# Kernel tuning notes

Hardware: AMD Instinct MI355X
Metric: run time of the kernel (lower is better)

Reference implementation:

```python
import jax, jax.numpy as jnp
import numpy as np

S = 4  # spixel_downsize


def _shift2d(x, oy, ox):
    # out[..., y, x] = x[..., y - oy, x - ox] if in-bounds else 0 (zero pad)
    pad = [(0, 0)] * (x.ndim - 2) + [(S, S), (S, S)]
    xp = jnp.pad(x, pad)
    h, w = x.shape[-2], x.shape[-1]
    return xp[..., S - oy:S - oy + h, S - ox:S - ox + w]


def _valid_mask(h, w, oy, ox):
    ys = jnp.arange(h)
    xs = jnp.arange(w)
    my = (ys - oy >= 0) & (ys - oy < h)
    mx = (xs - ox >= 0) & (xs - ox < w)
    return my[:, None] & mx[None, :]


def _conv3d(x, w, stride, pad):
    return jax.lax.conv_general_dilated(
        x, w, window_strides=stride, padding=[(p, p) for p in pad],
        dimension_numbers=('NCDHW', 'OIDHW', 'NCDHW'))


def _basic(x, w, stride, pad):
    # BasicConv: Conv3d(bias=False) + BN(identity at init) + ReLU
    return jax.nn.relu(_conv3d(x, w, stride, pad))


def setup_inputs() -> dict:
    key = jax.random.key(0)
    ks = jax.random.split(key, 8)
    cv = jax.random.normal(ks[0], (1, 8, 24, 128, 256), jnp.float32)
    sp = jax.random.uniform(ks[1], (1, 9, 128, 256), jnp.float32)
    xy = jax.random.normal(ks[2], (1, 2, 128, 256), jnp.float32)
    w_stem = jax.random.normal(ks[3], (16, 72, 1, 1, 1), jnp.float32) * 0.05
    w1a = jax.random.normal(ks[4], (32, 16, 3, 2, 2), jnp.float32) * 0.05
    w1b = jax.random.normal(ks[5], (32, 32, 3, 1, 1), jnp.float32) * 0.05
    w2a = jax.random.normal(ks[6], (64, 32, 3, 2, 2), jnp.float32) * 0.05
    w2b = jax.random.normal(ks[7], (64, 64, 3, 1, 1), jnp.float32) * 0.05
    return dict(cv=cv, sp=sp, xy=xy, w_stem=w_stem, w1a=w1a, w1b=w1b, w2a=w2a, w2b=w2b)


def reference(cv, sp, xy, w_stem, w1a, w1b, w2a, w2b):
    b, c, d, h, w = cv.shape
    feats, probs = [], []
    uv0 = jnp.zeros((b, 2, h, w), cv.dtype)
    # 9 shifted neighbors; neighbor k shifts by (S*((k//3)-1), S*((k%3)-1)).
    # All uv writes in the original target slot 0 and sequentially overwrite;
    for k in range(9):
        oy = S * ((k // 3) - 1)
        ox = S * ((k % 3) - 1)
        p = _shift2d(sp[:, k], oy, ox)                      # (b,h,w), zeros outside
        probs.append(p)
        feats.append(_shift2d(cv, oy, ox) * p[:, None, None])  # (b,c,d,h,w)
        u = _shift2d(xy, oy, ox) * p[:, None]               # (b,2,h,w)
        mask = _valid_mask(h, w, oy, ox)[None, None]
        uv0 = jnp.where(mask, u, uv0)
    # (b, c, 9, d, h, w) -> (b, 9c, d, h, w), matching torch reshape order
    feat = jnp.stack(feats, axis=2).reshape(b, c * 9, d, h, w)
    prob_sum = jnp.sum(jnp.stack(probs, axis=1), axis=1, keepdims=True)  # (b,1,h,w)
    tot = prob_sum.reshape(b, 1, h // S, S, w // S, S).mean((3, 5))      # avg_pool2d
    tot_up = jnp.repeat(jnp.repeat(tot, S, axis=2), S, axis=3)           # nearest upsample
    feat = feat / tot_up[:, :, None]                                     # (b,9c,d,h,w)
    feat = _basic(feat, w_stem, (1, 1, 1), (0, 0, 0))
    f1 = _basic(feat, w1a, (2, 2, 2), (1, 0, 0))
    f1 = _basic(f1, w1b, (1, 1, 1), (1, 0, 0))
    f2 = _basic(f1, w2a, (2, 2, 2), (1, 0, 0))
    f2 = _basic(f2, w2b, (1, 1, 1), (1, 0, 0))
    # uv.sum(2) == uv0 since only neighbor-slot 0 is written
    uv = uv0.reshape(b, 2, h // S, S, w // S, S).mean((3, 5)) / tot      # (b,2,h/S,w/S)
    return f1, f2, uv.reshape(b, 2, -1)
```

## Files before the change

### kernel.cpp

```cpp
#include <hip/hip_runtime.h>

#define HH 128
#define WW 256

#define OFF_TOT   0
#define OFF_WT    2048
#define WT_STEM   0
#define WT_1A     1152
#define WT_1B     7296
#define WT_2A     10368
#define WT_2B     34944
#define OFF_STEM  49280
#define OFF_F1A   12632192
#define OFF_F1N   15777920
#define OFF_F2A   49280

__global__ __launch_bounds__(256) void k_pre(
    const float* __restrict__ sp, const float* __restrict__ xy,
    const float* __restrict__ wstem, const float* __restrict__ w1a,
    const float* __restrict__ w1b, const float* __restrict__ w2a,
    const float* __restrict__ w2b,
    float* __restrict__ tot, float* __restrict__ uv_out, float* __restrict__ wt)
{
  int gid = blockIdx.x * 256 + threadIdx.x;
  if (gid < 1152) { int o = gid & 15, r = gid >> 4; int ci = r / 9, k = r - ci * 9;
    wt[WT_STEM + gid] = wstem[o * 72 + ci * 9 + k]; }
  if (gid < 6144) { int o = gid & 31, ci = (gid >> 5) & 15, tp = gid >> 9;
    wt[WT_1A + gid] = w1a[o * 192 + ci * 12 + tp]; }
  if (gid < 3072) { int o = gid & 31, ci = (gid >> 5) & 31, kd = gid >> 10;
    wt[WT_1B + gid] = w1b[(o * 32 + ci) * 3 + kd]; }
  if (gid < 24576) { int o = gid & 63, ci = (gid >> 6) & 31, tp = gid >> 11;
    wt[WT_2A + gid] = w2a[o * 384 + ci * 12 + tp]; }
  if (gid < 12288) { int o = gid & 63, ci = (gid >> 6) & 63, kd = gid >> 12;
    wt[WT_2B + gid] = w2b[(o * 64 + ci) * 3 + kd]; }
  if (gid < 8192) {
    int cell = gid >> 2, q = gid & 3;
    int Y = cell >> 6, X = cell & 63;
    float tsum = 0.f, u0 = 0.f, u1 = 0.f;
    int y = Y * 4 + q;
#pragma unroll
    for (int j = 0; j < 4; ++j) {
      int x = X * 4 + j;
      float psum = 0.f;
#pragma unroll
      for (int k = 0; k < 9; ++k) {
        int oy = 4 * ((k / 3) - 1), ox = 4 * ((k % 3) - 1);
        int sy = y - oy, sx = x - ox;
        if (sy >= 0 && sy < HH && sx >= 0 && sx < WW)
          psum += sp[k * HH * WW + sy * WW + sx];
      }
      tsum += psum;
      int oy = (y >= 4) ? 4 : 0;
      int ox = (x >= 4) ? 4 : 0;
      int kk = (oy ? 2 : 1) * 3 + (ox ? 2 : 1);
      int sy = y - oy, sx = x - ox;
      float p = sp[kk * HH * WW + sy * WW + sx];
      u0 += xy[sy * WW + sx] * p;
      u1 += xy[HH * WW + sy * WW + sx] * p;
    }
    tsum += __shfl_xor(tsum, 1); tsum += __shfl_xor(tsum, 2);
    u0 += __shfl_xor(u0, 1); u0 += __shfl_xor(u0, 2);
    u1 += __shfl_xor(u1, 1); u1 += __shfl_xor(u1, 2);
    if (q == 0) {
      float t = tsum * (1.f / 16.f);
      tot[cell] = t;
      float inv = 1.f / t;
      uv_out[cell] = u0 * (1.f / 16.f) * inv;
      uv_out[2048 + cell] = u1 * (1.f / 16.f) * inv;
    }
  }
}

__global__ __launch_bounds__(256) void k_stem(
    const float* __restrict__ cv, const float* __restrict__ sp,
    const float* __restrict__ wt, const float* __restrict__ tot,
    float* __restrict__ out)
{
  __shared__ float wl[1152];
  for (int i = threadIdx.x; i < 1152; i += 256) wl[i] = wt[i];
  __syncthreads();
  int x0 = blockIdx.x * 128 + 2 * (threadIdx.x & 63);
  int y  = blockIdx.y * 4 + (threadIdx.x >> 6);
  int d  = blockIdx.z;
  float2 p2[9]; int off[9];
#pragma unroll
  for (int k = 0; k < 9; ++k) {
    int oy = 4 * ((k / 3) - 1), ox = 4 * ((k % 3) - 1);
    int sy = y - oy, sx = x0 - ox;
    bool v = (sy >= 0) && (sy < HH) && (sx >= 0) && (sx < WW - 1);
    int syc = v ? sy : 0, sxc = v ? sx : 0;
    off[k] = syc * WW + sxc;
    float2 t = *(const float2*)(sp + k * HH * WW + off[k]);
    p2[k].x = v ? t.x : 0.f;
    p2[k].y = v ? t.y : 0.f;
  }
  float acc[16][2];
#pragma unroll
  for (int o = 0; o < 16; ++o) { acc[o][0] = 0.f; acc[o][1] = 0.f; }
  const float* cvd = cv + (size_t)d * HH * WW;
#pragma unroll
  for (int ci = 0; ci < 8; ++ci) {
    const float* cvp = cvd + (size_t)ci * 24 * HH * WW;
    float2 c2[9];
#pragma unroll
    for (int k = 0; k < 9; ++k) c2[k] = *(const float2*)(cvp + off[k]);
#pragma unroll
    for (int k = 0; k < 9; ++k) {
      float t0 = c2[k].x * p2[k].x, t1 = c2[k].y * p2[k].y;
      const float* wb = &wl[(ci * 9 + k) * 16];
      float wv[16];
#pragma unroll
      for (int q = 0; q < 4; ++q) *(float4*)&wv[q * 4] = *(const float4*)(wb + q * 4);
#pragma unroll
      for (int o = 0; o < 16; ++o) {
        acc[o][0] += wv[o] * t0;
        acc[o][1] += wv[o] * t1;
      }
    }
  }
  float inv = 1.f / tot[(y >> 2) * 64 + (x0 >> 2)];
  float* op = out + (((size_t)d * HH + y) * WW + x0) * 16;
#pragma unroll
  for (int p = 0; p < 2; ++p)
#pragma unroll
    for (int q = 0; q < 4; ++q) {
      float4 v;
      v.x = fmaxf(acc[q * 4 + 0][p] * inv, 0.f);
      v.y = fmaxf(acc[q * 4 + 1][p] * inv, 0.f);
      v.z = fmaxf(acc[q * 4 + 2][p] * inv, 0.f);
      v.w = fmaxf(acc[q * 4 + 3][p] * inv, 0.f);
      *(float4*)(op + p * 16 + q * 4) = v;
    }
}

__global__ __launch_bounds__(256) void k_conv1a(
    const float* __restrict__ in, const float* __restrict__ wt,
    float* __restrict__ out)
{
  __shared__ float wl[6144];
  for (int i = threadIdx.x; i < 6144; i += 256) wl[i] = wt[i];
  __syncthreads();
  int tid = threadIdx.x;
  int xo0 = (blockIdx.x & 1) * 64 + 2 * (tid & 31);
  int yo  = (blockIdx.x >> 1) * 8 + (tid >> 5);
  int dz = blockIdx.y, og = blockIdx.z;
  float acc[16][2];
#pragma unroll
  for (int o = 0; o < 16; ++o) { acc[o][0] = 0.f; acc[o][1] = 0.f; }
  for (int kd = 0; kd < 3; ++kd) {
    int d = 2 * dz - 1 + kd;
    if (d < 0 || d >= 24) continue;
#pragma unroll
    for (int ky = 0; ky < 2; ++ky) {
      int y = 2 * yo + ky;
      float iv[64];
      const float4* ip = (const float4*)(in + (((size_t)d * 128 + y) * 256 + 2 * xo0) * 16);
#pragma unroll
      for (int q = 0; q < 16; ++q) {
        float4 v = ip[q];
        iv[q * 4 + 0] = v.x; iv[q * 4 + 1] = v.y;
        iv[q * 4 + 2] = v.z; iv[q * 4 + 3] = v.w;
      }
#pragma unroll
      for (int kx = 0; kx < 2; ++kx) {
        const float* wtap = &wl[((kd * 2 + ky) * 2 + kx) * 512 + og * 16];
#pragma unroll
        for (int ci = 0; ci < 16; ++ci) {
          const float* wb = wtap + ci * 32;
          float wv[16];
#pragma unroll
          for (int q = 0; q < 4; ++q) *(float4*)&wv[q * 4] = *(const float4*)(wb + q * 4);
          float a0 = iv[(0 + kx) * 16 + ci];
          float a1 = iv[(2 + kx) * 16 + ci];
#pragma unroll
          for (int o = 0; o < 16; ++o) {
            acc[o][0] += wv[o] * a0;
            acc[o][1] += wv[o] * a1;
          }
        }
      }
    }
  }
  float* op = out + (((size_t)dz * 64 + yo) * 128 + xo0) * 32 + og * 16;
#pragma unroll
  for (int p = 0; p < 2; ++p)
#pragma unroll
    for (int q = 0; q < 4; ++q) {
      float4 v;
      v.x = fmaxf(acc[q * 4 + 0][p], 0.f);
      v.y = fmaxf(acc[q * 4 + 1][p], 0.f);
      v.z = fmaxf(acc[q * 4 + 2][p], 0.f);
      v.w = fmaxf(acc[q * 4 + 3][p], 0.f);
      *(float4*)(op + p * 32 + q * 4) = v;
    }
}

__global__ __launch_bounds__(256) void k_conv1b(
    const float* __restrict__ in, const float* __restrict__ wt,
    float* __restrict__ outn, float* __restrict__ outc)
{
  __shared__ float wl[3072];
  for (int i = threadIdx.x; i < 3072; i += 256) wl[i] = wt[i];
  __syncthreads();
  int tid = threadIdx.x;
  int xo = (blockIdx.x & 1) * 64 + (tid & 63);
  int yo = (blockIdx.x >> 1) * 4 + (tid >> 6);
  int dz = blockIdx.y, og = blockIdx.z;
  float acc[16];
#pragma unroll
  for (int o = 0; o < 16; ++o) acc[o] = 0.f;
  for (int kd = 0; kd < 3; ++kd) {
    int d = dz - 1 + kd;
    if (d < 0 || d >= 12) continue;
    float iv[32];
    const float4* ip = (const float4*)(in + (((size_t)d * 64 + yo) * 128 + xo) * 32);
#pragma unroll
    for (int q = 0; q < 8; ++q) {
      float4 v = ip[q];
      iv[q * 4 + 0] = v.x; iv[q * 4 + 1] = v.y;
      iv[q * 4 + 2] = v.z; iv[q * 4 + 3] = v.w;
    }
    const float* wk = &wl[kd * 1024 + og * 16];
#pragma unroll
    for (int ci = 0; ci < 32; ++ci) {
      const float* wb = wk + ci * 32;
      float wv[16];
#pragma unroll
      for (int q = 0; q < 4; ++q) *(float4*)&wv[q * 4] = *(const float4*)(wb + q * 4);
#pragma unroll
      for (int o = 0; o < 16; ++o) acc[o] += wv[o] * iv[ci];
    }
  }
  float* onp = outn + (((size_t)dz * 64 + yo) * 128 + xo) * 32 + og * 16;
#pragma unroll
  for (int q = 0; q < 4; ++q) {
    float4 v;
    v.x = fmaxf(acc[q * 4 + 0], 0.f);
    v.y = fmaxf(acc[q * 4 + 1], 0.f);
    v.z = fmaxf(acc[q * 4 + 2], 0.f);
    v.w = fmaxf(acc[q * 4 + 3], 0.f);
    *(float4*)(onp + q * 4) = v;
  }
#pragma unroll
  for (int o = 0; o < 16; ++o)
    outc[((size_t)((og * 16 + o) * 12 + dz) * 64 + yo) * 128 + xo] = fmaxf(acc[o], 0.f);
}

__global__ __launch_bounds__(256) void k_conv2a(
    const float* __restrict__ in, const float* __restrict__ wt,
    float* __restrict__ out)
{
  __shared__ float wl[3072];
  int og = blockIdx.z;
  for (int i = threadIdx.x; i < 3072; i += 256) {
    int o = i & 7, ci = (i >> 3) & 31, tap = i >> 8;
    wl[i] = wt[tap * 2048 + ci * 64 + og * 8 + o];
  }
  __syncthreads();
  int tid = threadIdx.x;
  int xo = tid & 63;
  int yo = blockIdx.x * 4 + (tid >> 6);
  int dz = blockIdx.y;
  float acc[8];
#pragma unroll
  for (int o = 0; o < 8; ++o) acc[o] = 0.f;
  for (int kd = 0; kd < 3; ++kd) {
    int d = 2 * dz - 1 + kd;
    if (d < 0 || d >= 12) continue;
#pragma unroll
    for (int ky = 0; ky < 2; ++ky) {
      int y = 2 * yo + ky;
      float iv[64];
      const float4* ip = (const float4*)(in + (((size_t)d * 64 + y) * 128 + 2 * xo) * 32);
#pragma unroll
      for (int q = 0; q < 16; ++q) {
        float4 v = ip[q];
        iv[q * 4 + 0] = v.x; iv[q * 4 + 1] = v.y;
        iv[q * 4 + 2] = v.z; iv[q * 4 + 3] = v.w;
      }
#pragma unroll
      for (int kx = 0; kx < 2; ++kx) {
        const float* wtap = &wl[((kd * 2 + ky) * 2 + kx) * 256];
#pragma unroll
        for (int ci = 0; ci < 32; ++ci) {
          const float* wb = wtap + ci * 8;
          float wv[8];
          *(float4*)&wv[0] = *(const float4*)(wb);
          *(float4*)&wv[4] = *(const float4*)(wb + 4);
          float a = iv[kx * 32 + ci];
#pragma unroll
          for (int o = 0; o < 8; ++o) acc[o] += wv[o] * a;
        }
      }
    }
  }
  float* op = out + (((size_t)dz * 32 + yo) * 64 + xo) * 64 + og * 8;
  float4 v0, v1;
  v0.x = fmaxf(acc[0], 0.f); v0.y = fmaxf(acc[1], 0.f);
  v0.z = fmaxf(acc[2], 0.f); v0.w = fmaxf(acc[3], 0.f);
  v1.x = fmaxf(acc[4], 0.f); v1.y = fmaxf(acc[5], 0.f);
  v1.z = fmaxf(acc[6], 0.f); v1.w = fmaxf(acc[7], 0.f);
  *(float4*)op = v0; *(float4*)(op + 4) = v1;
}

__global__ __launch_bounds__(256) void k_conv2b(
    const float* __restrict__ in, const float* __restrict__ wt,
    float* __restrict__ out)
{
  __shared__ float wl[1536];
  int og = blockIdx.z;
  for (int i = threadIdx.x; i < 1536; i += 256) {
    int o = i & 7, ci = (i >> 3) & 63, kd = i >> 9;
    wl[i] = wt[kd * 4096 + ci * 64 + og * 8 + o];
  }
  __syncthreads();
  int tid = threadIdx.x;
  int xo = tid & 63;
  int yo = blockIdx.x * 4 + (tid >> 6);
  int dz = blockIdx.y;
  float acc[8];
#pragma unroll
  for (int o = 0; o < 8; ++o) acc[o] = 0.f;
  for (int kd = 0; kd < 3; ++kd) {
    int d = dz - 1 + kd;
    if (d < 0 || d >= 6) continue;
    float iv[64];
    const float4* ip = (const float4*)(in + (((size_t)d * 32 + yo) * 64 + xo) * 64);
#pragma unroll
    for (int q = 0; q < 16; ++q) {
      float4 v = ip[q];
      iv[q * 4 + 0] = v.x; iv[q * 4 + 1] = v.y;
      iv[q * 4 + 2] = v.z; iv[q * 4 + 3] = v.w;
    }
    const float* wk = &wl[kd * 512];
#pragma unroll
    for (int ci = 0; ci < 64; ++ci) {
      const float* wb = wk + ci * 8;
      float wv[8];
      *(float4*)&wv[0] = *(const float4*)(wb);
      *(float4*)&wv[4] = *(const float4*)(wb + 4);
#pragma unroll
      for (int o = 0; o < 8; ++o) acc[o] += wv[o] * iv[ci];
    }
  }
#pragma unroll
  for (int o = 0; o < 8; ++o)
    out[((size_t)((og * 8 + o) * 6 + dz) * 32 + yo) * 64 + xo] = fmaxf(acc[o], 0.f);
}

extern "C" void kernel_launch(void* const* d_in, const int* in_sizes, int n_in,
                              void* d_out, int out_size, void* d_ws, size_t ws_size,
                              hipStream_t stream) {
  const float* cv    = (const float*)d_in[0];
  const float* sp    = (const float*)d_in[1];
  const float* xy    = (const float*)d_in[2];
  const float* wstem = (const float*)d_in[3];
  const float* w1a   = (const float*)d_in[4];
  const float* w1b   = (const float*)d_in[5];
  const float* w2a   = (const float*)d_in[6];
  const float* w2b   = (const float*)d_in[7];
  float* out = (float*)d_out;
  float* out_f1 = out;
  float* out_f2 = out + 3145728;
  float* out_uv = out + 3145728 + 786432;

  float* ws = (float*)d_ws;
  float* t_tot  = ws + OFF_TOT;
  float* wt     = ws + OFF_WT;
  float* t_stem = ws + OFF_STEM;
  float* t_f1a  = ws + OFF_F1A;
  float* t_f1n  = ws + OFF_F1N;
  float* t_f2a  = ws + OFF_F2A;

  k_pre<<<96, 256, 0, stream>>>(sp, xy, wstem, w1a, w1b, w2a, w2b,
                                t_tot, out_uv, wt);
  k_stem<<<dim3(2, 32, 24), 256, 0, stream>>>(cv, sp, wt + WT_STEM, t_tot, t_stem);
  k_conv1a<<<dim3(16, 12, 2), 256, 0, stream>>>(t_stem, wt + WT_1A, t_f1a);
  k_conv1b<<<dim3(32, 12, 2), 256, 0, stream>>>(t_f1a, wt + WT_1B, t_f1n, out_f1);
  k_conv2a<<<dim3(8, 6, 8), 256, 0, stream>>>(t_f1n, wt + WT_2A, t_f2a);
  k_conv2b<<<dim3(8, 6, 8), 256, 0, stream>>>(t_f2a, wt + WT_2B, out_f2);
}
```

Measured before the change: 174.7 us.

## Widen conv1a per-thread output tile and double-buffer stem channel loads

conv1a now has each thread compute four output x positions instead of two. Its shared weights are repacked to hold only this block's output-channel group, and the grid is halved in x. This raises FMA work per weight load from shared memory, at the cost of more accumulator registers (64) and fewer blocks. The stem kernel prefetches the next channel's cost-volume values into a register double buffer to hide global load latency. Other kernels get only cosmetic renames.

```diff
diff --git a/kernel.cpp b/kernel.cpp
--- a/kernel.cpp
+++ b/kernel.cpp
@@ -2,6 +2,7 @@
 
 #define HH 128
 #define WW 256
+#define HW (HH * WW)
 
 #define OFF_TOT   0
 #define OFF_WT    2048
@@ -47,16 +48,16 @@
         int oy = 4 * ((k / 3) - 1), ox = 4 * ((k % 3) - 1);
         int sy = y - oy, sx = x - ox;
         if (sy >= 0 && sy < HH && sx >= 0 && sx < WW)
-          psum += sp[k * HH * WW + sy * WW + sx];
+          psum += sp[k * HW + sy * WW + sx];
       }
       tsum += psum;
       int oy = (y >= 4) ? 4 : 0;
       int ox = (x >= 4) ? 4 : 0;
       int kk = (oy ? 2 : 1) * 3 + (ox ? 2 : 1);
       int sy = y - oy, sx = x - ox;
-      float p = sp[kk * HH * WW + sy * WW + sx];
+      float p = sp[kk * HW + sy * WW + sx];
       u0 += xy[sy * WW + sx] * p;
-      u1 += xy[HH * WW + sy * WW + sx] * p;
+      u1 += xy[HW + sy * WW + sx] * p;
     }
     tsum += __shfl_xor(tsum, 1); tsum += __shfl_xor(tsum, 2);
     u0 += __shfl_xor(u0, 1); u0 += __shfl_xor(u0, 2);
@@ -90,23 +91,28 @@
     bool v = (sy >= 0) && (sy < HH) && (sx >= 0) && (sx < WW - 1);
     int syc = v ? sy : 0, sxc = v ? sx : 0;
     off[k] = syc * WW + sxc;
-    float2 t = *(const float2*)(sp + k * HH * WW + off[k]);
+    float2 t = *(const float2*)(sp + k * HW + off[k]);
     p2[k].x = v ? t.x : 0.f;
     p2[k].y = v ? t.y : 0.f;
   }
   float acc[16][2];
 #pragma unroll
   for (int o = 0; o < 16; ++o) { acc[o][0] = 0.f; acc[o][1] = 0.f; }
-  const float* cvd = cv + (size_t)d * HH * WW;
+  const float* cvd = cv + (size_t)d * HW;
+  float2 cb[2][9];
+#pragma unroll
+  for (int k = 0; k < 9; ++k) cb[0][k] = *(const float2*)(cvd + off[k]);
 #pragma unroll
   for (int ci = 0; ci < 8; ++ci) {
-    const float* cvp = cvd + (size_t)ci * 24 * HH * WW;
-    float2 c2[9];
-#pragma unroll
-    for (int k = 0; k < 9; ++k) c2[k] = *(const float2*)(cvp + off[k]);
+    if (ci < 7) {
+#pragma unroll
+      for (int k = 0; k < 9; ++k)
+        cb[(ci + 1) & 1][k] = *(const float2*)(cvd + (size_t)(ci + 1) * 24 * HW + off[k]);
+    }
 #pragma unroll
     for (int k = 0; k < 9; ++k) {
-      float t0 = c2[k].x * p2[k].x, t1 = c2[k].y * p2[k].y;
+      float t0 = cb[ci & 1][k].x * p2[k].x;
+      float t1 = cb[ci & 1][k].y * p2[k].y;
       const float* wb = &wl[(ci * 9 + k) * 16];
       float wv[16];
 #pragma unroll
@@ -137,53 +143,67 @@
     const float* __restrict__ in, const float* __restrict__ wt,
     float* __restrict__ out)
 {
-  __shared__ float wl[6144];
-  for (int i = threadIdx.x; i < 6144; i += 256) wl[i] = wt[i];
-  __syncthreads();
-  int tid = threadIdx.x;
-  int xo0 = (blockIdx.x & 1) * 64 + 2 * (tid & 31);
-  int yo  = (blockIdx.x >> 1) * 8 + (tid >> 5);
-  int dz = blockIdx.y, og = blockIdx.z;
-  float acc[16][2];
-#pragma unroll
-  for (int o = 0; o < 16; ++o) { acc[o][0] = 0.f; acc[o][1] = 0.f; }
+  __shared__ float wl[3072];
+  int og = blockIdx.z;
+  for (int i = threadIdx.x; i < 3072; i += 256) {
+    int o = i & 15, ci = (i >> 4) & 15, tap = i >> 8;
+    wl[i] = wt[tap * 512 + ci * 32 + og * 16 + o];
+  }
+  __syncthreads();
+  int tx = threadIdx.x & 31;
+  int ty = threadIdx.x >> 5;
+  int yo = blockIdx.x * 8 + ty;
+  int dz = blockIdx.y;
+  float acc[16][4];
+#pragma unroll
+  for (int o = 0; o < 16; ++o)
+#pragma unroll
+    for (int p = 0; p < 4; ++p) acc[o][p] = 0.f;
   for (int kd = 0; kd < 3; ++kd) {
     int d = 2 * dz - 1 + kd;
     if (d < 0 || d >= 24) continue;
 #pragma unroll
     for (int ky = 0; ky < 2; ++ky) {
       int y = 2 * yo + ky;
-      float iv[64];
-      const float4* ip = (const float4*)(in + (((size_t)d * 128 + y) * 256 + 2 * xo0) * 16);
-#pragma unroll
-      for (int q = 0; q < 16; ++q) {
-        float4 v = ip[q];
-        iv[q * 4 + 0] = v.x; iv[q * 4 + 1] = v.y;
-        iv[q * 4 + 2] = v.z; iv[q * 4 + 3] = v.w;
-      }
+      const float* base = in + (((size_t)d * 128 + y) * 256 + 8 * tx) * 16;
 #pragma unroll
       for (int kx = 0; kx < 2; ++kx) {
-        const float* wtap = &wl[((kd * 2 + ky) * 2 + kx) * 512 + og * 16];
+        float ib[64];
+#pragma unroll
+        for (int p = 0; p < 4; ++p) {
+          const float4* ip = (const float4*)(base + (2 * p + kx) * 16);
+#pragma unroll
+          for (int q = 0; q < 4; ++q) {
+            float4 t = ip[q];
+            ib[p * 16 + q * 4 + 0] = t.x; ib[p * 16 + q * 4 + 1] = t.y;
+            ib[p * 16 + q * 4 + 2] = t.z; ib[p * 16 + q * 4 + 3] = t.w;
+          }
+        }
+        const float* wtap = &wl[((kd * 2 + ky) * 2 + kx) * 256];
 #pragma unroll
         for (int ci = 0; ci < 16; ++ci) {
-          const float* wb = wtap + ci * 32;
           float wv[16];
 #pragma unroll
-          for (int q = 0; q < 4; ++q) *(float4*)&wv[q * 4] = *(const float4*)(wb + q * 4);
-          float a0 = iv[(0 + kx) * 16 + ci];
-          float a1 = iv[(2 + kx) * 16 + ci];
+          for (int q = 0; q < 4; ++q)
+            *(float4*)&wv[q * 4] = *(const float4*)(wtap + ci * 16 + q * 4);
+          float a0 = ib[0 * 16 + ci];
+          float a1 = ib[1 * 16 + ci];
+          float a2 = ib[2 * 16 + ci];
+          float a3 = ib[3 * 16 + ci];
 #pragma unroll
           for (int o = 0; o < 16; ++o) {
             acc[o][0] += wv[o] * a0;
             acc[o][1] += wv[o] * a1;
+            acc[o][2] += wv[o] * a2;
+            acc[o][3] += wv[o] * a3;
           }
         }
       }
     }
   }
-  float* op = out + (((size_t)dz * 64 + yo) * 128 + xo0) * 32 + og * 16;
-#pragma unroll
-  for (int p = 0; p < 2; ++p)
+  float* op = out + (((size_t)dz * 64 + yo) * 128 + 4 * tx) * 32 + og * 16;
+#pragma unroll
+  for (int p = 0; p < 4; ++p)
 #pragma unroll
     for (int q = 0; q < 4; ++q) {
       float4 v;
@@ -257,9 +277,8 @@
     wl[i] = wt[tap * 2048 + ci * 64 + og * 8 + o];
   }
   __syncthreads();
-  int tid = threadIdx.x;
-  int xo = tid & 63;
-  int yo = blockIdx.x * 4 + (tid >> 6);
+  int xo = threadIdx.x & 63;
+  int yo = blockIdx.x * 4 + (threadIdx.x >> 6);
   int dz = blockIdx.y;
   float acc[8];
 #pragma unroll
@@ -270,13 +289,12 @@
 #pragma unroll
     for (int ky = 0; ky < 2; ++ky) {
       int y = 2 * yo + ky;
-      float iv[64];
+      float ib[64];
       const float4* ip = (const float4*)(in + (((size_t)d * 64 + y) * 128 + 2 * xo) * 32);
 #pragma unroll
       for (int q = 0; q < 16; ++q) {
-        float4 v = ip[q];
-        iv[q * 4 + 0] = v.x; iv[q * 4 + 1] = v.y;
-        iv[q * 4 + 2] = v.z; iv[q * 4 + 3] = v.w;
+        float4 t = ip[q];
+        ib[q * 4] = t.x; ib[q * 4 + 1] = t.y; ib[q * 4 + 2] = t.z; ib[q * 4 + 3] = t.w;
       }
 #pragma unroll
       for (int kx = 0; kx < 2; ++kx) {
@@ -285,9 +303,9 @@
         for (int ci = 0; ci < 32; ++ci) {
           const float* wb = wtap + ci * 8;
           float wv[8];
-          *(float4*)&wv[0] = *(const float4*)(wb);
+          *(float4*)&wv[0] = *(const float4*)wb;
           *(float4*)&wv[4] = *(const float4*)(wb + 4);
-          float a = iv[kx * 32 + ci];
+          float a = ib[kx * 32 + ci];
 #pragma unroll
           for (int o = 0; o < 8; ++o) acc[o] += wv[o] * a;
         }
@@ -314,9 +332,8 @@
     wl[i] = wt[kd * 4096 + ci * 64 + og * 8 + o];
   }
   __syncthreads();
-  int tid = threadIdx.x;
-  int xo = tid & 63;
-  int yo = blockIdx.x * 4 + (tid >> 6);
+  int xo = threadIdx.x & 63;
+  int yo = blockIdx.x * 4 + (threadIdx.x >> 6);
   int dz = blockIdx.y;
   float acc[8];
 #pragma unroll
@@ -324,23 +341,23 @@
   for (int kd = 0; kd < 3; ++kd) {
     int d = dz - 1 + kd;
     if (d < 0 || d >= 6) continue;
-    float iv[64];
+    float ib[64];
     const float4* ip = (const float4*)(in + (((size_t)d * 32 + yo) * 64 + xo) * 64);
 #pragma unroll
     for (int q = 0; q < 16; ++q) {
-      float4 v = ip[q];
-      iv[q * 4 + 0] = v.x; iv[q * 4 + 1] = v.y;
-      iv[q * 4 + 2] = v.z; iv[q * 4 + 3] = v.w;
+      float4 t = ip[q];
+      ib[q * 4] = t.x; ib[q * 4 + 1] = t.y; ib[q * 4 + 2] = t.z; ib[q * 4 + 3] = t.w;
     }
     const float* wk = &wl[kd * 512];
 #pragma unroll
     for (int ci = 0; ci < 64; ++ci) {
       const float* wb = wk + ci * 8;
       float wv[8];
-      *(float4*)&wv[0] = *(const float4*)(wb);
+      *(float4*)&wv[0] = *(const float4*)wb;
       *(float4*)&wv[4] = *(const float4*)(wb + 4);
-#pragma unroll
-      for (int o = 0; o < 8; ++o) acc[o] += wv[o] * iv[ci];
+      float a = ib[ci];
+#pragma unroll
+      for (int o = 0; o < 8; ++o) acc[o] += wv[o] * a;
     }
   }
 #pragma unroll
@@ -375,7 +392,7 @@
   k_pre<<<96, 256, 0, stream>>>(sp, xy, wstem, w1a, w1b, w2a, w2b,
                                 t_tot, out_uv, wt);
   k_stem<<<dim3(2, 32, 24), 256, 0, stream>>>(cv, sp, wt + WT_STEM, t_tot, t_stem);
-  k_conv1a<<<dim3(16, 12, 2), 256, 0, stream>>>(t_stem, wt + WT_1A, t_f1a);
+  k_conv1a<<<dim3(8, 12, 2), 256, 0, stream>>>(t_stem, wt + WT_1A, t_f1a);
   k_conv1b<<<dim3(32, 12, 2), 256, 0, stream>>>(t_f1a, wt + WT_1B, t_f1n, out_f1);
   k_conv2a<<<dim3(8, 6, 8), 256, 0, stream>>>(t_f1n, wt + WT_2A, t_f2a);
   k_conv2b<<<dim3(8, 6, 8), 256, 0, stream>>>(t_f2a, wt + WT_2B, out_f2);
```

Result: no change. 172.2 us, median of 2 (-1.4%).
